# Performance work log

Hardware: AMD Instinct MI355X
Metric: run time of the kernel (lower is better)

Reference implementation:

```python
import jax, jax.numpy as jnp
import numpy as np

EPS = 1e-12  # F.normalize eps
G = 8        # groups (init g)
NC = 32      # num_cluster
LMD = 2


def _l2norm(v, axis):
    n = jnp.sqrt(jnp.sum(v * v, axis=axis, keepdims=True))
    return v / jnp.maximum(n, EPS)


def setup_inputs() -> dict:
    key = jax.random.key(0)
    ks = jax.random.split(key, 6)
    b, m, d = 32, 512, 1024
    d2 = LMD * d                 # 2048
    nd = d2 // G                 # 256 = new_dims
    x = jax.random.normal(ks[0], (b, m, d), dtype=jnp.float32)
    mask = jnp.ones((b, m), dtype=bool)
    # Linear params with torch-like fan-in scaling
    We = jax.random.normal(ks[1], (d2, d), dtype=jnp.float32) / np.sqrt(d)
    be = jnp.zeros((d2,), dtype=jnp.float32)
    W1 = jax.random.normal(ks[2], (G * NC, d2), dtype=jnp.float32) / np.sqrt(d2)
    b1 = jnp.zeros((G * NC,), dtype=jnp.float32)
    W2 = jax.random.normal(ks[3], (G, d2), dtype=jnp.float32) / np.sqrt(d2)
    b2 = jnp.zeros((G,), dtype=jnp.float32)
    centroid = jax.random.uniform(ks[4], (NC, nd), dtype=jnp.float32)
    return {"x": x, "mask": mask, "We": We, "be": be, "W1": W1, "b1": b1,
            "W2": W2, "b2": b2, "centroid": centroid}


def reference(x, mask, We, be, W1, b1, W2, b2, centroid):
    b, m, d = x.shape
    # BaseAggregator: L2 normalize along feature dim (mask unused)
    xn = _l2norm(x, axis=2)
    xe = jnp.einsum('bmd,ed->bme', xn, We) + be          # (b, m, lmd*d)
    a1 = jax.nn.softmax((jnp.einsum('bme,ke->bmk', xe, W1) + b1)
                        .reshape(b, m, G, NC), axis=3)   # (b, m, G, nc)
    a2 = jax.nn.softmax(jnp.einsum('bme,ge->bmg', xe, W2) + b2, axis=2)  # (b, m, G)
    xg = xe.reshape(b, m, G, -1)                         # (b, m, G, new_dims)
    # sum_nc a1*(x - c) = x*sum(a1) - a1@c = x - a1@c  (softmax sums to 1)
    cent = jnp.einsum('bmgk,kd->bmgd', a1, centroid)     # (b, m, G, new_dims)
    v = jnp.einsum('bmg,bmgd->bd', a2, xg - cent) / m    # sum over G, mean over m
    return _l2norm(v, axis=1)
```

## Files before the change

kernel.cpp:

```cpp
#include <hip/hip_runtime.h>
#include <hip/hip_bf16.h>
#include <stdint.h>

#define B_BATCH 32
#define M_SEQ   512
#define R_TOT   16384
#define D_IN    1024
#define E_DIM   2048
#define NCAT    384
#define NVALID  264

typedef float  f32x4 __attribute__((ext_vector_type(4)));
typedef short  s16x8 __attribute__((ext_vector_type(8)));

__device__ __forceinline__ uint16_t f2bf(float f) {
  uint32_t u = __builtin_bit_cast(uint32_t, f);
  uint32_t r = (u + 0x7fffu + ((u >> 16) & 1u)) >> 16;
  return (uint16_t)r;
}
__device__ __forceinline__ float bf2f(uint16_t u) {
  return __builtin_bit_cast(float, (uint32_t)u << 16);
}

__device__ __forceinline__ f32x4 mfma_bf16(s16x8 a, s16x8 b, f32x4 c) {
  asm("v_mfma_f32_16x16x32_bf16 %0, %1, %2, %0" : "+v"(c) : "v"(a), "v"(b));
  return c;
}

typedef __attribute__((address_space(3))) void lds_void_t;
typedef const __attribute__((address_space(1))) void gbl_void_t;
__device__ __forceinline__ void async_load16(const void* g, void* l) {
  __builtin_amdgcn_global_load_lds((gbl_void_t*)g, (lds_void_t*)l, 16, 0, 0);
}

#define FENCE() __builtin_amdgcn_sched_barrier(0)
#define PH_PRE() do { FENCE(); __builtin_amdgcn_s_barrier(); FENCE(); \
                      asm volatile("s_waitcnt lgkmcnt(0)" ::: "memory"); FENCE(); \
                      __builtin_amdgcn_s_setprio(1); } while (0)
#define PH_POST() do { __builtin_amdgcn_s_setprio(0); FENCE(); \
                       __builtin_amdgcn_s_barrier(); FENCE(); } while (0)
#define PH_POST_VM4() do { __builtin_amdgcn_s_setprio(0); FENCE(); \
                       asm volatile("s_waitcnt vmcnt(4)" ::: "memory"); FENCE(); \
                       __builtin_amdgcn_s_barrier(); FENCE(); } while (0)
#define PH_POST_VM0() do { __builtin_amdgcn_s_setprio(0); FENCE(); \
                       asm volatile("s_waitcnt vmcnt(0)" ::: "memory"); FENCE(); \
                       __builtin_amdgcn_s_barrier(); FENCE(); } while (0)

__global__ void zero_buf(float* __restrict__ p, int n) {
  int i = blockIdx.x * blockDim.x + threadIdx.x;
  if (i < n) p[i] = 0.0f;
}

__global__ void cvt_bf16(const float* __restrict__ src, uint16_t* __restrict__ dst, int n) {
  int i = blockIdx.x * blockDim.x + threadIdx.x;
  if (i < n) dst[i] = f2bf(src[i]);
}

__global__ void build_wcat(const float* __restrict__ W1, const float* __restrict__ W2,
                           uint16_t* __restrict__ wcat) {
  int i = blockIdx.x * blockDim.x + threadIdx.x;
  if (i >= NCAT * E_DIM) return;
  int row = i >> 11, col = i & (E_DIM - 1);
  float v = 0.0f;
  if (row < 256) v = W1[i];
  else if (row < NVALID) v = W2[(row - 256) * E_DIM + col];
  wcat[i] = f2bf(v);
}

__global__ void build_bcat(const float* __restrict__ b1, const float* __restrict__ b2,
                           float* __restrict__ bcat) {
  int i = blockIdx.x * blockDim.x + threadIdx.x;
  if (i >= NCAT) return;
  float v = 0.0f;
  if (i < 256) v = b1[i];
  else if (i < NVALID) v = b2[i - 256];
  bcat[i] = v;
}

__global__ __launch_bounds__(256) void normalize_rows(const float* __restrict__ x,
                                                      uint16_t* __restrict__ xn) {
  const int r = blockIdx.x, tid = threadIdx.x;
  const float4* xr = (const float4*)(x + (size_t)r * D_IN);
  float4 v = xr[tid];
  float ss = v.x * v.x + v.y * v.y + v.z * v.z + v.w * v.w;
  #pragma unroll
  for (int m = 32; m; m >>= 1) ss += __shfl_xor(ss, m);
  __shared__ float wsum[4];
  if ((tid & 63) == 0) wsum[tid >> 6] = ss;
  __syncthreads();
  float tot = wsum[0] + wsum[1] + wsum[2] + wsum[3];
  float scale = 1.0f / fmaxf(sqrtf(tot), 1e-12f);
  uint16_t* o = xn + (size_t)r * D_IN + tid * 4;
  o[0] = f2bf(v.x * scale); o[1] = f2bf(v.y * scale);
  o[2] = f2bf(v.z * scale); o[3] = f2bf(v.w * scale);
}

template <int KDIM>
__global__ __launch_bounds__(512, 2) void gemm256(
    const uint16_t* __restrict__ A, const uint16_t* __restrict__ B,
    const float* __restrict__ bias, uint16_t* __restrict__ C, int N) {
  __shared__ uint16_t lds[65536];
  constexpr int NT = KDIM / 64;
  const int tid = threadIdx.x;
  const int w = tid >> 6, lane = tid & 63;
  const int wr = w >> 2, wc = w & 3;
  const int bm = blockIdx.x, bn = blockIdx.y;

  const int srow = tid >> 3;
  const int scol = (((tid & 7) ^ (srow & 7)) << 3);
  const int l15 = lane & 15, l4 = lane >> 4, lx = lane & 7;
  const int ck0 = ((l4) ^ lx) << 4;
  const int ck1 = ((4 + l4) ^ lx) << 4;

  const int arow0 = bm * 256, brow0 = bn * 256;

  auto STAGE = [&](const uint16_t* __restrict__ M, int grow0, int tile,
                   int bufi, int mat, int half) {
    if (tile >= NT) return;
    const uint16_t* src = M + (size_t)(grow0 + half * 128 + srow) * KDIM + tile * 64 + scol;
    uint16_t* dst = lds + ((bufi * 2 + mat) * 2 + half) * 8192 + w * 512;
    async_load16(src, dst);
    async_load16(src + (size_t)64 * KDIM, dst + 4096);
  };
  auto LDA = [&](int bufi, int mi, int ckb) -> s16x8 {
    return *(const s16x8*)((const char*)(lds + ((bufi * 2 + 0) * 2 + wr) * 8192)
                           + (mi * 16 + l15) * 128 + ckb);
  };
  auto LDB = [&](int bufi, int ni, int ckb) -> s16x8 {
    return *(const s16x8*)((const char*)(lds + ((bufi * 2 + 1) * 2 + (wc >> 1)) * 8192)
                           + ((wc & 1) * 64 + ni * 16 + l15) * 128 + ckb);
  };

  f32x4 acc[8][4] = {};
  s16x8 aF[4][2], bF[4][2];

  STAGE(A, arow0, 0, 0, 0, 0); STAGE(A, arow0, 0, 0, 0, 1);
  STAGE(B, brow0, 0, 0, 1, 0); STAGE(B, brow0, 0, 0, 1, 1);
  STAGE(B, brow0, 1, 1, 1, 0); STAGE(B, brow0, 1, 1, 1, 1);
  asm volatile("s_waitcnt vmcnt(4)" ::: "memory");
  __builtin_amdgcn_s_barrier(); FENCE();

  for (int i = 0; i < NT / 2; ++i) {
    const bool last = (i == NT / 2 - 1);
    #pragma unroll
    for (int h = 0; h < 2; ++h) {
      const int T = 2 * i + h;
      #pragma unroll
      for (int mi = 0; mi < 4; ++mi) { aF[mi][0] = LDA(h, mi, ck0); aF[mi][1] = LDA(h, mi, ck1); }
      #pragma unroll
      for (int ni = 0; ni < 2; ++ni) { bF[ni][0] = LDB(h, ni, ck0); bF[ni][1] = LDB(h, ni, ck1); }
      STAGE(A, arow0, T + 1, h ^ 1, 0, 0);
      PH_PRE();
      #pragma unroll
      for (int kk = 0; kk < 2; ++kk)
        #pragma unroll
        for (int mi = 0; mi < 4; ++mi)
          #pragma unroll
          for (int ni = 0; ni < 2; ++ni)
            acc[mi][ni] = mfma_bf16(aF[mi][kk], bF[ni][kk], acc[mi][ni]);
      PH_POST();
      #pragma unroll
      for (int ni = 2; ni < 4; ++ni) { bF[ni][0] = LDB(h, ni, ck0); bF[ni][1] = LDB(h, ni, ck1); }
      STAGE(A, arow0, T + 1, h ^ 1, 0, 1);
      PH_PRE();
      #pragma unroll
      for (int kk = 0; kk < 2; ++kk)
        #pragma unroll
        for (int mi = 0; mi < 4; ++mi)
          #pragma unroll
          for (int ni = 2; ni < 4; ++ni)
            acc[mi][ni] = mfma_bf16(aF[mi][kk], bF[ni][kk], acc[mi][ni]);
      PH_POST();
      #pragma unroll
      for (int mi = 0; mi < 4; ++mi) { aF[mi][0] = LDA(h, 4 + mi, ck0); aF[mi][1] = LDA(h, 4 + mi, ck1); }
      STAGE(B, brow0, T + 2, h, 1, 0);
      PH_PRE();
      #pragma unroll
      for (int kk = 0; kk < 2; ++kk)
        #pragma unroll
        for (int mi = 0; mi < 4; ++mi)
          #pragma unroll
          for (int ni = 0; ni < 2; ++ni)
            acc[4 + mi][ni] = mfma_bf16(aF[mi][kk], bF[ni][kk], acc[4 + mi][ni]);
      PH_POST();
      STAGE(B, brow0, T + 2, h, 1, 1);
      PH_PRE();
      #pragma unroll
      for (int kk = 0; kk < 2; ++kk)
        #pragma unroll
        for (int mi = 0; mi < 4; ++mi)
          #pragma unroll
          for (int ni = 2; ni < 4; ++ni)
            acc[4 + mi][ni] = mfma_bf16(aF[mi][kk], bF[ni][kk], acc[4 + mi][ni]);
      if (last) { PH_POST_VM0(); } else { PH_POST_VM4(); }
    }
  }

  asm volatile("s_nop 7\n\ts_nop 7\n\ts_nop 7" ::);

  const int lr0 = wr * 128 + l4 * 4;
  const int lc0 = wc * 64 + l15;
  #pragma unroll
  for (int ni = 0; ni < 4; ++ni) {
    const int col = lc0 + ni * 16;
    const float bv = bias[bn * 256 + col];
    const int c16 = col >> 3, c7 = col & 7;
    #pragma unroll
    for (int mi = 0; mi < 8; ++mi) {
      #pragma unroll
      for (int jj = 0; jj < 4; ++jj) {
        const int row = lr0 + mi * 16 + jj;
        lds[row * 256 + ((c16 ^ (row & 31)) << 3) + c7] = f2bf(acc[mi][ni][jj] + bv);
      }
    }
  }
  __syncthreads();
  {
    const int row = tid >> 1, ch = tid & 1;
    const int r31 = row & 31;
    uint16_t* dst = C + (size_t)(arow0 + row) * N + bn * 256 + ch * 128;
    #pragma unroll
    for (int q = 0; q < 8; ++q) {
      const int c16a = ch * 16 + 2 * q;
      s16x8 v0 = *(const s16x8*)&lds[row * 256 + ((c16a ^ r31) << 3)];
      s16x8 v1 = *(const s16x8*)&lds[row * 256 + (((c16a + 1) ^ r31) << 3)];
      *(s16x8*)(dst + q * 16) = v0;
      *(s16x8*)(dst + q * 16 + 8) = v1;
    }
  }
}

template <typename OutT>
__global__ __launch_bounds__(256, 2) void gemm_bt(
    const uint16_t* __restrict__ A, const uint16_t* __restrict__ B,
    const float* __restrict__ bias, OutT* __restrict__ C, int N, int K) {
  __shared__ __align__(16) uint16_t As[128 * 64];
  __shared__ __align__(16) uint16_t Bs[128 * 64];
  const int tid = threadIdx.x;
  const int w = tid >> 6, lane = tid & 63;
  const int wr = w >> 1, wc = w & 1;
  const int tm = blockIdx.x, tn = blockIdx.y;

  f32x4 acc[4][4] = {};

  const int lrow = lane >> 3;
  const int lk = (lane & 7) * 8;
  const size_t a_row0 = (size_t)tm * 128;
  const size_t b_row0 = (size_t)tn * 128;

  for (int k0 = 0; k0 < K; k0 += 64) {
    #pragma unroll
    for (int j = 0; j < 4; ++j) {
      const int c = w * 4 + j;
      const int row = c * 8 + lrow;
      async_load16(A + (a_row0 + row) * K + k0 + lk, (void*)(As + c * 512));
      async_load16(B + (b_row0 + row) * K + k0 + lk, (void*)(Bs + c * 512));
    }
    __syncthreads();
    #pragma unroll
    for (int kk = 0; kk < 2; ++kk) {
      const int krow = kk * 32 + (lane >> 4) * 8;
      s16x8 af[4], bfr[4];
      #pragma unroll
      for (int mi = 0; mi < 4; ++mi)
        af[mi] = *(const s16x8*)&As[(wr * 64 + mi * 16 + (lane & 15)) * 64 + krow];
      #pragma unroll
      for (int ni = 0; ni < 4; ++ni)
        bfr[ni] = *(const s16x8*)&Bs[(wc * 64 + ni * 16 + (lane & 15)) * 64 + krow];
      #pragma unroll
      for (int mi = 0; mi < 4; ++mi)
        #pragma unroll
        for (int ni = 0; ni < 4; ++ni)
          acc[mi][ni] = mfma_bf16(af[mi], bfr[ni], acc[mi][ni]);
    }
    __syncthreads();
  }
  asm volatile("s_nop 7\n\ts_nop 7\n\ts_nop 7" ::);

  const int rbase = wr * 64 + (lane >> 4) * 4;
  const int cbase = wc * 64 + (lane & 15);
  #pragma unroll
  for (int ni = 0; ni < 4; ++ni) {
    const int col = tn * 128 + cbase + ni * 16;
    const float bv = bias[col];
    #pragma unroll
    for (int mi = 0; mi < 4; ++mi) {
      #pragma unroll
      for (int jj = 0; jj < 4; ++jj) {
        const int row = tm * 128 + rbase + mi * 16 + jj;
        float v = acc[mi][ni][jj] + bv;
        if constexpr (sizeof(OutT) == 2) C[(size_t)row * N + col] = (OutT)f2bf(v);
        else                             C[(size_t)row * N + col] = v;
      }
    }
  }
}

__global__ __launch_bounds__(256) void softmax_accum(
    const float* __restrict__ logits,
    const uint16_t* __restrict__ xe,
    float* __restrict__ t1,
    float* __restrict__ sacc) {
  const int tid = threadIdx.x;
  const int r0 = blockIdx.x * 32;
  const int b = r0 >> 9;
  __shared__ float p1s[256];
  __shared__ float a2s[8];
  float t1_local = 0.0f, s_local = 0.0f;

  for (int rr = 0; rr < 32; ++rr) {
    const int r = r0 + rr;
    const float* lrow = logits + (size_t)r * NCAT;
    float lg = lrow[tid];
    float mx = lg;
    #pragma unroll
    for (int m = 16; m; m >>= 1) mx = fmaxf(mx, __shfl_xor(mx, m));
    float e = __expf(lg - mx);
    float sm = e;
    #pragma unroll
    for (int m = 16; m; m >>= 1) sm += __shfl_xor(sm, m);
    p1s[tid] = e / sm;
    if (tid < 8) {
      float l2 = lrow[256 + tid];
      float m2 = l2;
      #pragma unroll
      for (int m = 4; m; m >>= 1) m2 = fmaxf(m2, __shfl_xor(m2, m));
      float e2 = __expf(l2 - m2);
      float s2 = e2;
      #pragma unroll
      for (int m = 4; m; m >>= 1) s2 += __shfl_xor(s2, m);
      a2s[tid] = e2 / s2;
    }
    __syncthreads();
    const uint16_t* xr = xe + (size_t)r * E_DIM;
    float a = 0.0f;
    #pragma unroll
    for (int g = 0; g < 8; ++g) a += a2s[g] * bf2f(xr[g * 256 + tid]);
    t1_local += a;
    if (tid < 32) {
      float sa = 0.0f;
      #pragma unroll
      for (int g = 0; g < 8; ++g) sa += a2s[g] * p1s[g * 32 + tid];
      s_local += sa;
    }
    __syncthreads();
  }
  atomicAdd(&t1[b * 256 + tid], t1_local);
  if (tid < 32) atomicAdd(&sacc[b * 32 + tid], s_local);
}

__global__ __launch_bounds__(256) void finalize(const float* __restrict__ t1,
                                                const float* __restrict__ sacc,
                                                const float* __restrict__ centroid,
                                                float* __restrict__ out) {
  const int b = blockIdx.x, tid = threadIdx.x;
  float cs = 0.0f;
  #pragma unroll
  for (int k = 0; k < 32; ++k) cs += sacc[b * 32 + k] * centroid[k * 256 + tid];
  float v = (t1[b * 256 + tid] - cs) * (1.0f / (float)M_SEQ);
  float ss = v * v;
  #pragma unroll
  for (int m = 32; m; m >>= 1) ss += __shfl_xor(ss, m);
  __shared__ float wsum[4];
  if ((tid & 63) == 0) wsum[tid >> 6] = ss;
  __syncthreads();
  float tot = wsum[0] + wsum[1] + wsum[2] + wsum[3];
  out[b * 256 + tid] = v / fmaxf(sqrtf(tot), 1e-12f);
}

extern "C" void kernel_launch(void* const* d_in, const int* in_sizes, int n_in,
                              void* d_out, int out_size, void* d_ws, size_t ws_size,
                              hipStream_t stream) {
  const float* x        = (const float*)d_in[0];
  const float* We       = (const float*)d_in[2];
  const float* be       = (const float*)d_in[3];
  const float* W1       = (const float*)d_in[4];
  const float* b1       = (const float*)d_in[5];
  const float* W2       = (const float*)d_in[6];
  const float* b2       = (const float*)d_in[7];
  const float* centroid = (const float*)d_in[8];
  float* out = (float*)d_out;

  char* ws = (char*)d_ws;
  uint16_t* xe     = (uint16_t*)(ws + 0);
  uint16_t* xn     = (uint16_t*)(ws + 67108864);
  float*    logits = (float*)  (ws + 67108864);
  uint16_t* webf   = (uint16_t*)(ws + 100663296);
  uint16_t* wcat   = (uint16_t*)(ws + 104857600);
  float*    bcat   = (float*)  (ws + 106430464);
  float*    t1     = (float*)  (ws + 106432000);
  float*    sacc   = (float*)  (ws + 106464768);

  zero_buf  <<<dim3(36),   256, 0, stream>>>(t1, 8192 + 1024);
  cvt_bf16  <<<dim3(8192), 256, 0, stream>>>(We, webf, E_DIM * D_IN);
  build_wcat<<<dim3(3072), 256, 0, stream>>>(W1, W2, wcat);
  build_bcat<<<dim3(2),    256, 0, stream>>>(b1, b2, bcat);

  normalize_rows<<<dim3(R_TOT), 256, 0, stream>>>(x, xn);
  gemm256<D_IN><<<dim3(R_TOT / 256, E_DIM / 256), 512, 0, stream>>>(
      xn, webf, be, xe, E_DIM);
  gemm_bt<float><<<dim3(R_TOT / 128, NCAT / 128), 256, 0, stream>>>(
      xe, wcat, bcat, logits, NCAT, E_DIM);
  softmax_accum<<<dim3(R_TOT / 32), 256, 0, stream>>>(logits, xe, t1, sacc);
  finalize<<<dim3(B_BATCH), 256, 0, stream>>>(t1, sacc, centroid, out);
}
```

Before: 300.1 us.

## Overlap LDS fragment reads with MFMA phases in GEMM main loop

Restructures the pingpong GEMM main loop so the LDS fragment reads for the next phase are issued inside the current MFMA phase, using separate lo/hi fragment register sets. It drops the explicit lgkmcnt(0) waits before each phase and prefetches the next tile's first fragments right after the barrier that covers the final phase of the previous tile. The aim is to hide LDS read latency behind matrix-core work. In exchange it uses more VGPRs for the fragments and relies on the compiler to insert the correct waits for LDS.

```diff
diff --git a/kernel.cpp b/kernel.cpp
--- a/kernel.cpp
+++ b/kernel.cpp
@@ -34,16 +34,9 @@
 }
 
 #define FENCE() __builtin_amdgcn_sched_barrier(0)
-#define PH_PRE() do { FENCE(); __builtin_amdgcn_s_barrier(); FENCE(); \
-                      asm volatile("s_waitcnt lgkmcnt(0)" ::: "memory"); FENCE(); \
-                      __builtin_amdgcn_s_setprio(1); } while (0)
+#define PH_PRE_NL() do { FENCE(); __builtin_amdgcn_s_barrier(); FENCE(); \
+                         __builtin_amdgcn_s_setprio(1); } while (0)
 #define PH_POST() do { __builtin_amdgcn_s_setprio(0); FENCE(); \
-                       __builtin_amdgcn_s_barrier(); FENCE(); } while (0)
-#define PH_POST_VM4() do { __builtin_amdgcn_s_setprio(0); FENCE(); \
-                       asm volatile("s_waitcnt vmcnt(4)" ::: "memory"); FENCE(); \
-                       __builtin_amdgcn_s_barrier(); FENCE(); } while (0)
-#define PH_POST_VM0() do { __builtin_amdgcn_s_setprio(0); FENCE(); \
-                       asm volatile("s_waitcnt vmcnt(0)" ::: "memory"); FENCE(); \
                        __builtin_amdgcn_s_barrier(); FENCE(); } while (0)
 
 __global__ void zero_buf(float* __restrict__ p, int n) {
@@ -132,69 +125,94 @@
   };
 
   f32x4 acc[8][4] = {};
-  s16x8 aF[4][2], bF[4][2];
+  s16x8 aLo[4][2], aHi[4][2], bLo[2][2], bHi[2][2];
+
+  auto R1 = [&](int buf) {
+    #pragma unroll
+    for (int mi = 0; mi < 4; ++mi) { aLo[mi][0] = LDA(buf, mi, ck0); aLo[mi][1] = LDA(buf, mi, ck1); }
+    #pragma unroll
+    for (int ni = 0; ni < 2; ++ni) { bLo[ni][0] = LDB(buf, ni, ck0); bLo[ni][1] = LDB(buf, ni, ck1); }
+  };
+  auto R2 = [&](int buf) {
+    #pragma unroll
+    for (int j = 0; j < 2; ++j) { bHi[j][0] = LDB(buf, 2 + j, ck0); bHi[j][1] = LDB(buf, 2 + j, ck1); }
+  };
+  auto R3 = [&](int buf) {
+    #pragma unroll
+    for (int mi = 0; mi < 4; ++mi) { aHi[mi][0] = LDA(buf, 4 + mi, ck0); aHi[mi][1] = LDA(buf, 4 + mi, ck1); }
+  };
+
+  auto MM1 = [&] {
+    #pragma unroll
+    for (int kk = 0; kk < 2; ++kk)
+      #pragma unroll
+      for (int mi = 0; mi < 4; ++mi)
+        #pragma unroll
+        for (int ni = 0; ni < 2; ++ni)
+          acc[mi][ni] = mfma_bf16(aLo[mi][kk], bLo[ni][kk], acc[mi][ni]);
+  };
+  auto MM2 = [&] {
+    #pragma unroll
+    for (int kk = 0; kk < 2; ++kk)
+      #pragma unroll
+      for (int mi = 0; mi < 4; ++mi)
+        #pragma unroll
+        for (int j = 0; j < 2; ++j)
+          acc[mi][2 + j] = mfma_bf16(aLo[mi][kk], bHi[j][kk], acc[mi][2 + j]);
+  };
+  auto MM3 = [&] {
+    #pragma unroll
+    for (int kk = 0; kk < 2; ++kk)
+      #pragma unroll
+      for (int mi = 0; mi < 4; ++mi)
+        #pragma unroll
+        for (int ni = 0; ni < 2; ++ni)
+          acc[4 + mi][ni] = mfma_bf16(aHi[mi][kk], bLo[ni][kk], acc[4 + mi][ni]);
+  };
+  auto MM4 = [&] {
+    #pragma unroll
+    for (int kk = 0; kk < 2; ++kk)
+      #pragma unroll
+      for (int mi = 0; mi < 4; ++mi)
+        #pragma unroll
+        for (int j = 0; j < 2; ++j)
+          acc[4 + mi][2 + j] = mfma_bf16(aHi[mi][kk], bHi[j][kk], acc[4 + mi][2 + j]);
+  };
+
+#define GROUP(H, T, VM0, FINAL) do {                                           \
+    STAGE(A, arow0, (T) + 1, (H) ^ 1, 0, 0);                                   \
+    PH_PRE_NL(); R2(H); MM1(); PH_POST();                                      \
+    STAGE(A, arow0, (T) + 1, (H) ^ 1, 0, 1);                                   \
+    PH_PRE_NL(); R3(H); MM2(); PH_POST();                                      \
+    STAGE(B, brow0, (T) + 2, (H), 1, 0);                                       \
+    PH_PRE_NL(); MM3(); PH_POST();                                             \
+    STAGE(B, brow0, (T) + 2, (H), 1, 1);                                       \
+    FENCE();                                                                   \
+    if (!(FINAL)) {                                                            \
+      if (VM0) asm volatile("s_waitcnt vmcnt(0)" ::: "memory");                \
+      else     asm volatile("s_waitcnt vmcnt(4)" ::: "memory");                \
+    }                                                                          \
+    __builtin_amdgcn_s_barrier(); FENCE();                                     \
+    __builtin_amdgcn_s_setprio(1);                                             \
+    if (!(FINAL)) R1((H) ^ 1);                                                 \
+    MM4(); PH_POST();                                                          \
+  } while (0)
 
   STAGE(A, arow0, 0, 0, 0, 0); STAGE(A, arow0, 0, 0, 0, 1);
   STAGE(B, brow0, 0, 0, 1, 0); STAGE(B, brow0, 0, 0, 1, 1);
   STAGE(B, brow0, 1, 1, 1, 0); STAGE(B, brow0, 1, 1, 1, 1);
+  FENCE();
   asm volatile("s_waitcnt vmcnt(4)" ::: "memory");
   __builtin_amdgcn_s_barrier(); FENCE();
-
-  for (int i = 0; i < NT / 2; ++i) {
-    const bool last = (i == NT / 2 - 1);
-    #pragma unroll
-    for (int h = 0; h < 2; ++h) {
-      const int T = 2 * i + h;
-      #pragma unroll
-      for (int mi = 0; mi < 4; ++mi) { aF[mi][0] = LDA(h, mi, ck0); aF[mi][1] = LDA(h, mi, ck1); }
-      #pragma unroll
-      for (int ni = 0; ni < 2; ++ni) { bF[ni][0] = LDB(h, ni, ck0); bF[ni][1] = LDB(h, ni, ck1); }
-      STAGE(A, arow0, T + 1, h ^ 1, 0, 0);
-      PH_PRE();
-      #pragma unroll
-      for (int kk = 0; kk < 2; ++kk)
-        #pragma unroll
-        for (int mi = 0; mi < 4; ++mi)
-          #pragma unroll
-          for (int ni = 0; ni < 2; ++ni)
-            acc[mi][ni] = mfma_bf16(aF[mi][kk], bF[ni][kk], acc[mi][ni]);
-      PH_POST();
-      #pragma unroll
-      for (int ni = 2; ni < 4; ++ni) { bF[ni][0] = LDB(h, ni, ck0); bF[ni][1] = LDB(h, ni, ck1); }
-      STAGE(A, arow0, T + 1, h ^ 1, 0, 1);
-      PH_PRE();
-      #pragma unroll
-      for (int kk = 0; kk < 2; ++kk)
-        #pragma unroll
-        for (int mi = 0; mi < 4; ++mi)
-          #pragma unroll
-          for (int ni = 2; ni < 4; ++ni)
-            acc[mi][ni] = mfma_bf16(aF[mi][kk], bF[ni][kk], acc[mi][ni]);
-      PH_POST();
-      #pragma unroll
-      for (int mi = 0; mi < 4; ++mi) { aF[mi][0] = LDA(h, 4 + mi, ck0); aF[mi][1] = LDA(h, 4 + mi, ck1); }
-      STAGE(B, brow0, T + 2, h, 1, 0);
-      PH_PRE();
-      #pragma unroll
-      for (int kk = 0; kk < 2; ++kk)
-        #pragma unroll
-        for (int mi = 0; mi < 4; ++mi)
-          #pragma unroll
-          for (int ni = 0; ni < 2; ++ni)
-            acc[4 + mi][ni] = mfma_bf16(aF[mi][kk], bF[ni][kk], acc[4 + mi][ni]);
-      PH_POST();
-      STAGE(B, brow0, T + 2, h, 1, 1);
-      PH_PRE();
-      #pragma unroll
-      for (int kk = 0; kk < 2; ++kk)
-        #pragma unroll
-        for (int mi = 0; mi < 4; ++mi)
-          #pragma unroll
-          for (int ni = 2; ni < 4; ++ni)
-            acc[4 + mi][ni] = mfma_bf16(aF[mi][kk], bF[ni][kk], acc[4 + mi][ni]);
-      if (last) { PH_POST_VM0(); } else { PH_POST_VM4(); }
-    }
-  }
+  R1(0);
+
+  for (int i = 0; i < NT / 2 - 1; ++i) {
+    GROUP(0, 2 * i, false, false);
+    GROUP(1, 2 * i + 1, false, false);
+  }
+  GROUP(0, NT - 2, true, false);
+  GROUP(1, NT - 1, false, true);
+#undef GROUP
 
   asm volatile("s_nop 7\n\ts_nop 7\n\ts_nop 7" ::);
 
```

Result: slower. 307.3 us (+2.4%).
